# Optimization experiments

Hardware: AMD Instinct MI355X
Metric: run time of the kernel (lower is better)

The kernel has to match this reference:

```python
import jax, jax.numpy as jnp
import numpy as np

N, F_IN, C, H, E, G = 10000, 128, 256, 4, 160000, 512
BN_EPS = 1e-5


def setup_inputs() -> dict:
    key = jax.random.key(0)
    ks = iter(jax.random.split(key, 40))
    nrm = lambda shape, s=0.05: jax.random.normal(next(ks), shape, jnp.float32) * s

    def bn(dim):
        # rows: gamma, beta, running_mean, running_var (eval-mode BatchNorm)
        g = 1.0 + jax.random.normal(next(ks), (dim,), jnp.float32) * 0.1
        b = jax.random.normal(next(ks), (dim,), jnp.float32) * 0.1
        m = jax.random.normal(next(ks), (dim,), jnp.float32) * 0.1
        v = jax.random.uniform(next(ks), (dim,), jnp.float32, 0.5, 1.5)
        return jnp.stack([g, b, m, v])  # [4, dim]

    x = jax.random.normal(next(ks), (N, F_IN), jnp.float32)
    edge_index = jax.random.randint(next(ks), (2, E), 0, N, jnp.int64)
    batch = (jnp.arange(N, dtype=jnp.int64) * G) // N  # sorted, every graph non-empty

    return {
        "x": x, "edge_index": edge_index, "batch": batch,
        "W1": nrm((F_IN, H * C)), "att_src1": nrm((H, C)), "att_dst1": nrm((H, C)), "b1": nrm((H * C,)), "bn1": bn(H * C),
        "W2": nrm((H * C, H * C)), "att_src2": nrm((H, C)), "att_dst2": nrm((H, C)), "b2": nrm((H * C,)), "bn2": bn(H * C),
        "W3": nrm((H * C, C)), "att_src3": nrm((1, C)), "att_dst3": nrm((1, C)), "b3": nrm((C,)), "bn3": bn(C),
        "fc1_w": nrm((3 * C, 2 * C)), "fc1_b": nrm((2 * C,)), "bnf1": bn(2 * C),
        "fc2_w": nrm((2 * C, C)), "fc2_b": nrm((C,)), "bnf2": bn(C),
        "fc3_w": nrm((C, 1)), "fc3_b": nrm((1,)),
    }


def batchnorm(x, p):
    g, b, m, v = p
    return (x - m) * (g * jax.lax.rsqrt(v + BN_EPS)) + b


def gat_conv(x, src, dst, W, att_src, att_dst, bias, heads):
    n = x.shape[0]
    h = (x @ W).reshape(n, heads, -1)                      # [N,H,C]
    a_src = jnp.einsum('nhc,hc->nh', h, att_src)           # [N,H]
    a_dst = jnp.einsum('nhc,hc->nh', h, att_dst)
    logits = jax.nn.leaky_relu(a_src[src] + a_dst[dst], 0.2)  # [E,H]
    # scatter-softmax over incoming edges of each destination node
    m = jax.ops.segment_max(logits, dst, num_segments=n)
    m = jax.lax.stop_gradient(jnp.where(jnp.isfinite(m), m, 0.0))
    e = jnp.exp(logits - m[dst])
    denom = jax.ops.segment_sum(e, dst, num_segments=n)
    alpha = e / (denom[dst] + 1e-16)                       # [E,H]
    msg = h[src] * alpha[:, :, None]                       # [E,H,C]
    out = jax.ops.segment_sum(msg, dst, num_segments=n)    # [N,H,C]
    return out.reshape(n, -1) + bias


def reference(x, edge_index, batch,
              W1, att_src1, att_dst1, b1, bn1,
              W2, att_src2, att_dst2, b2, bn2,
              W3, att_src3, att_dst3, b3, bn3,
              fc1_w, fc1_b, bnf1, fc2_w, fc2_b, bnf2, fc3_w, fc3_b):
    src, dst = edge_index[0], edge_index[1]
    h = jax.nn.elu(batchnorm(gat_conv(x, src, dst, W1, att_src1, att_dst1, b1, H), bn1))
    h = jax.nn.elu(batchnorm(gat_conv(h, src, dst, W2, att_src2, att_dst2, b2, H), bn2))
    h = jax.nn.elu(batchnorm(gat_conv(h, src, dst, W3, att_src3, att_dst3, b3, 1), bn3))
    # multi-pool readout over graphs
    s = jax.ops.segment_sum(h, batch, num_segments=G)
    cnt = jax.ops.segment_sum(jnp.ones((h.shape[0], 1), h.dtype), batch, num_segments=G)
    mean = s / cnt
    mx = jax.ops.segment_max(h, batch, num_segments=G)
    z = jnp.concatenate([mean, mx, s], axis=1)             # [G, 3C]
    z = jax.nn.relu(batchnorm(z @ fc1_w + fc1_b, bnf1))    # dropout: eval mode (identity)
    z = jax.nn.relu(batchnorm(z @ fc2_w + fc2_b, bnf2))
    return z @ fc3_w + fc3_b                               # [G, 1]
```

## Files before the change

kernel.cpp:

```cpp
#include <hip/hip_runtime.h>
#include <math.h>

#define N_NODES 10000
#define N_EDGES 160000
#define N_GRAPH 512

#define NEG_INF (-1e30f)

typedef __attribute__((ext_vector_type(8))) short s16x8;
typedef __attribute__((ext_vector_type(4))) float f32x4;

__device__ __forceinline__ unsigned short f2b(float f) {
  union { float f; unsigned u; } c{f};
  unsigned u = c.u;
  return (unsigned short)((u + 0x7fff + ((u >> 16) & 1)) >> 16);
}
__device__ __forceinline__ float b2f(unsigned short h) {
  union { unsigned u; float f; } c{(unsigned)h << 16};
  return c.f;
}
__device__ __forceinline__ void up2(unsigned d, float& lo, float& hi) {
  union { unsigned u; float f; } a{d << 16}, b{d & 0xffff0000u};
  lo = a.f; hi = b.f;
}
__device__ __forceinline__ float lrelu(float x) { return x > 0.f ? x : 0.2f * x; }

#define GLL16(gp, lp)                                                          \
  __builtin_amdgcn_global_load_lds(                                            \
      (const __attribute__((address_space(1))) unsigned int*)(gp),             \
      (__attribute__((address_space(3))) unsigned int*)(lp), 16, 0, 0)

__global__ void k_count(const int* __restrict__ dst, const int* __restrict__ batch,
                        int* __restrict__ deg, int* __restrict__ gcnt) {
  int i = blockIdx.x * 256 + threadIdx.x;
  if (i < N_EDGES) atomicAdd(&deg[dst[i]], 1);
  if (i < N_NODES) atomicAdd(&gcnt[batch[i]], 1);
}

__global__ void k_scan2(const int* __restrict__ in1, int* __restrict__ out1, int n1,
                        const int* __restrict__ in2, int* __restrict__ out2, int n2) {
  __shared__ int buf[1024];
  __shared__ int carry_s;
#pragma unroll 1
  for (int pass = 0; pass < 2; ++pass) {
    const int* in = pass ? in2 : in1;
    int* out = pass ? out2 : out1;
    const int n = pass ? n2 : n1;
    if (threadIdx.x == 0) carry_s = 0;
    __syncthreads();
    for (int base = 0; base < n; base += 1024) {
      int i = base + (int)threadIdx.x;
      int v = (i < n) ? in[i] : 0;
      buf[threadIdx.x] = v;
      __syncthreads();
      for (int off = 1; off < 1024; off <<= 1) {
        int t = (threadIdx.x >= (unsigned)off) ? buf[threadIdx.x - off] : 0;
        __syncthreads();
        buf[threadIdx.x] += t;
        __syncthreads();
      }
      int carry = carry_s;
      if (i < n) out[i] = carry + buf[threadIdx.x] - v;
      __syncthreads();
      if (threadIdx.x == 0) carry_s = carry + buf[1023];
      __syncthreads();
    }
    if (threadIdx.x == 0) out[n] = carry_s;
    __syncthreads();
  }
}

__global__ void k_fill(const int* __restrict__ src, const int* __restrict__ dst,
                       const int* __restrict__ rowoff, int* __restrict__ cursor,
                       int* __restrict__ csr) {
  int e = blockIdx.x * 256 + threadIdx.x;
  if (e < N_EDGES) {
    int d = dst[e];
    int p = atomicAdd(&cursor[d], 1);
    csr[rowoff[d] + p] = src[e];
  }
}

__global__ __launch_bounds__(256) void k_sortseg(const int* __restrict__ rowoff,
                                                 int* __restrict__ vals) {
  const int node = blockIdx.x * 4 + (threadIdx.x >> 6);
  if (node >= N_NODES) return;
  const int lane = threadIdx.x & 63;
  const int a = rowoff[node], b = rowoff[node + 1];
  const int deg = b - a;
  if (deg <= 1) return;
  if (deg <= 64) {
    int v = (lane < deg) ? vals[a + lane] : 0x7fffffff;
#pragma unroll
    for (int ph = 0; ph < 64; ++ph) {
      const int par = ph & 1;
      const bool left = ((lane & 1) == par);
      const int partner = left ? lane + 1 : lane - 1;
      const int pv = __shfl(v, partner & 63);
      if (partner >= 0 && partner < 64) v = left ? min(v, pv) : max(v, pv);
    }
    if (lane < deg) vals[a + lane] = v;
  } else if (lane == 0) {
    for (int p = a + 1; p < b; ++p) {
      int v = vals[p];
      int q = p - 1;
      while (q >= a && vals[q] > v) { vals[q + 1] = vals[q]; --q; }
      vals[q + 1] = v;
    }
  }
}

__global__ __launch_bounds__(256) void k_convT(const float* __restrict__ in,
                                               unsigned short* __restrict__ out,
                                               int K, int M) {
  __shared__ float t[32][33];
  const int mb = blockIdx.x * 32, kb = blockIdx.y * 32;
  const int tx = threadIdx.x & 31, ty = threadIdx.x >> 5;
#pragma unroll
  for (int r = ty; r < 32; r += 8) t[r][tx] = in[(size_t)(kb + r) * M + mb + tx];
  __syncthreads();
#pragma unroll
  for (int r = ty; r < 32; r += 8)
    out[(size_t)(mb + r) * K + kb + tx] = f2b(t[tx][r]);
}

__global__ void k_wmix(const float* __restrict__ W, const float* __restrict__ attS,
                       const float* __restrict__ attD, float* __restrict__ wS,
                       float* __restrict__ wD) {
  const int i = blockIdx.x * 256 + threadIdx.x;
  if (i >= 512) return;
  const int f = i >> 2, h = i & 3;
  const float* wrow = W + (size_t)f * 1024 + h * 256;
  const float* as = attS + h * 256;
  const float* ad = attD + h * 256;
  float s = 0.f, d = 0.f;
  for (int c = 0; c < 256; ++c) {
    const float w = wrow[c];
    s += w * as[c];
    d += w * ad[c];
  }
  wS[f * 4 + h] = s;
  wD[f * 4 + h] = d;
}

__global__ __launch_bounds__(256) void k_prep_x(const float* __restrict__ x,
                                                const float* __restrict__ wS,
                                                const float* __restrict__ wD,
                                                unsigned short* __restrict__ x_bf,
                                                float* __restrict__ aS,
                                                float* __restrict__ aD) {
  __shared__ float sS[128][4], sD[128][4];
  const int tid = threadIdx.x;
  for (int i = tid; i < 512; i += 256) {
    sS[i >> 2][i & 3] = wS[i];
    sD[i >> 2][i & 3] = wD[i];
  }
  __syncthreads();
  const int node = blockIdx.x * 4 + (tid >> 6);
  if (node >= N_NODES) return;
  const int lane = tid & 63;
  const float2 xv = ((const float2*)(x + (size_t)node * 128))[lane];
  const unsigned o = (unsigned)f2b(xv.x) | ((unsigned)f2b(xv.y) << 16);
  ((unsigned*)x_bf)[(size_t)node * 64 + lane] = o;
  const float4 s0 = *(const float4*)sS[lane * 2];
  const float4 s1 = *(const float4*)sS[lane * 2 + 1];
  const float4 d0 = *(const float4*)sD[lane * 2];
  const float4 d1 = *(const float4*)sD[lane * 2 + 1];
  float a0 = xv.x * s0.x + xv.y * s1.x;
  float a1 = xv.x * s0.y + xv.y * s1.y;
  float a2 = xv.x * s0.z + xv.y * s1.z;
  float a3 = xv.x * s0.w + xv.y * s1.w;
  float b0 = xv.x * d0.x + xv.y * d1.x;
  float b1 = xv.x * d0.y + xv.y * d1.y;
  float b2 = xv.x * d0.z + xv.y * d1.z;
  float b3 = xv.x * d0.w + xv.y * d1.w;
#pragma unroll
  for (int off = 32; off; off >>= 1) {
    a0 += __shfl_xor(a0, off); a1 += __shfl_xor(a1, off);
    a2 += __shfl_xor(a2, off); a3 += __shfl_xor(a3, off);
    b0 += __shfl_xor(b0, off); b1 += __shfl_xor(b1, off);
    b2 += __shfl_xor(b2, off); b3 += __shfl_xor(b3, off);
  }
  if (lane == 0) {
    *(float4*)&aS[(size_t)node * 4] = make_float4(a0, a1, a2, a3);
    *(float4*)&aD[(size_t)node * 4] = make_float4(b0, b1, b2, b3);
  }
}

__global__ __launch_bounds__(256) void k_aggx(
    const unsigned short* __restrict__ x_bf, const float* __restrict__ aS,
    const float* __restrict__ aD, const int* __restrict__ rowoff,
    const int* __restrict__ csr, unsigned short* __restrict__ xt) {
  const int wv = threadIdx.x >> 6;
  const int lane = threadIdx.x & 63;
  const int node = blockIdx.x * 4 + wv;
  if (node >= N_NODES) return;

  __shared__ int s_src_all[4][64];
  __shared__ float s_alp_all[4][64][4];
  int* s_src = s_src_all[wv];
  float (*s_alp)[4] = s_alp_all[wv];

  const int r0 = rowoff[node];
  const int deg = rowoff[node + 1] - r0;
  const float4 ad4 = *(const float4*)&aD[(size_t)node * 4];

  float acc[8];
#pragma unroll
  for (int j = 0; j < 8; ++j) acc[j] = 0.f;

  auto gather = [&](int cnt) {
    int e = 0;
    for (; e + 4 <= cnt; e += 4) {
      unsigned v[4];
      float4 al[4];
#pragma unroll
      for (int u = 0; u < 4; ++u) {
        const int s = s_src[e + u];
        al[u] = *(const float4*)s_alp[e + u];
        v[u] = ((const unsigned*)(x_bf + ((size_t)s << 7)))[lane];
      }
#pragma unroll
      for (int u = 0; u < 4; ++u) {
        float lo, hi;
        up2(v[u], lo, hi);
        acc[0] += al[u].x * lo; acc[1] += al[u].x * hi;
        acc[2] += al[u].y * lo; acc[3] += al[u].y * hi;
        acc[4] += al[u].z * lo; acc[5] += al[u].z * hi;
        acc[6] += al[u].w * lo; acc[7] += al[u].w * hi;
      }
    }
    for (; e < cnt; ++e) {
      const int s = s_src[e];
      const float4 al = *(const float4*)s_alp[e];
      const unsigned v = ((const unsigned*)(x_bf + ((size_t)s << 7)))[lane];
      float lo, hi;
      up2(v, lo, hi);
      acc[0] += al.x * lo; acc[1] += al.x * hi;
      acc[2] += al.y * lo; acc[3] += al.y * hi;
      acc[4] += al.z * lo; acc[5] += al.z * hi;
      acc[6] += al.w * lo; acc[7] += al.w * hi;
    }
  };

  if (deg <= 64) {
    float l0, l1, l2, l3;
    int sE = 0;
    const bool act = lane < deg;
    if (act) {
      sE = csr[r0 + lane];
      const float4 sv = *(const float4*)&aS[(size_t)sE * 4];
      l0 = lrelu(sv.x + ad4.x);
      l1 = lrelu(sv.y + ad4.y);
      l2 = lrelu(sv.z + ad4.z);
      l3 = lrelu(sv.w + ad4.w);
    } else {
      l0 = l1 = l2 = l3 = NEG_INF;
    }
    float m0 = l0, m1 = l1, m2 = l2, m3 = l3;
#pragma unroll
    for (int off = 32; off; off >>= 1) {
      m0 = fmaxf(m0, __shfl_xor(m0, off));
      m1 = fmaxf(m1, __shfl_xor(m1, off));
      m2 = fmaxf(m2, __shfl_xor(m2, off));
      m3 = fmaxf(m3, __shfl_xor(m3, off));
    }
    float e0 = act ? __expf(l0 - m0) : 0.f;
    float e1 = act ? __expf(l1 - m1) : 0.f;
    float e2 = act ? __expf(l2 - m2) : 0.f;
    float e3 = act ? __expf(l3 - m3) : 0.f;
    float s0 = e0, s1 = e1, s2 = e2, s3 = e3;
#pragma unroll
    for (int off = 32; off; off >>= 1) {
      s0 += __shfl_xor(s0, off);
      s1 += __shfl_xor(s1, off);
      s2 += __shfl_xor(s2, off);
      s3 += __shfl_xor(s3, off);
    }
    if (act) {
      s_src[lane] = sE;
      s_alp[lane][0] = e0 / (s0 + 1e-16f);
      s_alp[lane][1] = e1 / (s1 + 1e-16f);
      s_alp[lane][2] = e2 / (s2 + 1e-16f);
      s_alp[lane][3] = e3 / (s3 + 1e-16f);
    }
    gather(deg);
  } else {
    auto logits = [&](int idx, float& a, float& b, float& c, float& d, int& s) {
      s = csr[r0 + idx];
      const float4 sv = *(const float4*)&aS[(size_t)s * 4];
      a = lrelu(sv.x + ad4.x);
      b = lrelu(sv.y + ad4.y);
      c = lrelu(sv.z + ad4.z);
      d = lrelu(sv.w + ad4.w);
    };
    float m0 = NEG_INF, m1 = NEG_INF, m2 = NEG_INF, m3 = NEG_INF;
    for (int base = 0; base < deg; base += 64) {
      if (base + lane < deg) {
        float a, b, c, d; int s;
        logits(base + lane, a, b, c, d, s);
        m0 = fmaxf(m0, a); m1 = fmaxf(m1, b); m2 = fmaxf(m2, c); m3 = fmaxf(m3, d);
      }
    }
#pragma unroll
    for (int off = 32; off; off >>= 1) {
      m0 = fmaxf(m0, __shfl_xor(m0, off));
      m1 = fmaxf(m1, __shfl_xor(m1, off));
      m2 = fmaxf(m2, __shfl_xor(m2, off));
      m3 = fmaxf(m3, __shfl_xor(m3, off));
    }
    float s0 = 0.f, s1 = 0.f, s2 = 0.f, s3 = 0.f;
    for (int base = 0; base < deg; base += 64) {
      if (base + lane < deg) {
        float a, b, c, d; int s;
        logits(base + lane, a, b, c, d, s);
        s0 += __expf(a - m0); s1 += __expf(b - m1);
        s2 += __expf(c - m2); s3 += __expf(d - m3);
      }
    }
#pragma unroll
    for (int off = 32; off; off >>= 1) {
      s0 += __shfl_xor(s0, off);
      s1 += __shfl_xor(s1, off);
      s2 += __shfl_xor(s2, off);
      s3 += __shfl_xor(s3, off);
    }
    const float d0 = 1.f / (s0 + 1e-16f), d1 = 1.f / (s1 + 1e-16f);
    const float d2 = 1.f / (s2 + 1e-16f), d3 = 1.f / (s3 + 1e-16f);
    for (int base = 0; base < deg; base += 64) {
      const int cnt = min(64, deg - base);
      if (lane < cnt) {
        float a, b, c, d; int s;
        logits(base + lane, a, b, c, d, s);
        s_src[lane] = s;
        s_alp[lane][0] = __expf(a - m0) * d0;
        s_alp[lane][1] = __expf(b - m1) * d1;
        s_alp[lane][2] = __expf(c - m2) * d2;
        s_alp[lane][3] = __expf(d - m3) * d3;
      }
      gather(cnt);
    }
  }

#pragma unroll
  for (int h = 0; h < 4; ++h) {
    const unsigned o = (unsigned)f2b(acc[h * 2]) | ((unsigned)f2b(acc[h * 2 + 1]) << 16);
    ((unsigned*)xt)[(size_t)node * 256 + h * 64 + lane] = o;
  }
}

__global__ __launch_bounds__(256) void k_gemm_bf16(
    const unsigned short* __restrict__ A, int lda,
    const unsigned short* __restrict__ Bt, int ldb,
    unsigned short* __restrict__ Cbf, int ldc,
    int M, int N, int K) {
  __shared__ unsigned short As[128 * 32];
  __shared__ unsigned short Bs[128 * 32];
  const int tid = threadIdx.x;
  const int lane = tid & 63, wave = tid >> 6;
  const int wr = wave >> 1, wc = wave & 1;
  const int m0 = blockIdx.y * 128, n0 = blockIdx.x * 128;

  f32x4 acc[4][4];
#pragma unroll
  for (int i = 0; i < 4; ++i)
#pragma unroll
    for (int j = 0; j < 4; ++j) acc[i][j] = (f32x4){0.f, 0.f, 0.f, 0.f};

  const int l4 = lane >> 2;
  const int kp8 = (lane & 3) * 8;
  int rA0 = m0 + wave * 32 + l4;
  int rA1 = rA0 + 16;
  rA0 = min(rA0, M - 1);
  rA1 = min(rA1, M - 1);
  const int rB0 = n0 + wave * 32 + l4;
  const int rB1 = rB0 + 16;
  const unsigned short* pA0 = A + (size_t)rA0 * lda + kp8;
  const unsigned short* pA1 = A + (size_t)rA1 * lda + kp8;
  const unsigned short* pB0 = Bt + (size_t)rB0 * ldb + kp8;
  const unsigned short* pB1 = Bt + (size_t)rB1 * ldb + kp8;
  unsigned short* lA = As + wave * 1024;
  unsigned short* lB = Bs + wave * 1024;

  const int fr = lane & 15, kg = (lane >> 4) * 8;

  for (int kb = 0; kb < K; kb += 32) {
    GLL16(pA0 + kb, lA);
    GLL16(pA1 + kb, lA + 512);
    GLL16(pB0 + kb, lB);
    GLL16(pB1 + kb, lB + 512);
    __syncthreads();

    s16x8 a[4], b[4];
#pragma unroll
    for (int m = 0; m < 4; ++m)
      a[m] = *(const s16x8*)&As[(wr * 64 + m * 16 + fr) * 32 + kg];
#pragma unroll
    for (int n = 0; n < 4; ++n)
      b[n] = *(const s16x8*)&Bs[(wc * 64 + n * 16 + fr) * 32 + kg];
#pragma unroll
    for (int m = 0; m < 4; ++m)
#pragma unroll
      for (int n = 0; n < 4; ++n)
        acc[m][n] = __builtin_amdgcn_mfma_f32_16x16x32_bf16(a[m], b[n], acc[m][n], 0, 0, 0);
    __syncthreads();
  }

  const int frow = (lane >> 4) * 4;
#pragma unroll
  for (int m = 0; m < 4; ++m) {
#pragma unroll
    for (int r = 0; r < 4; ++r) {
      const int row = m0 + wr * 64 + m * 16 + frow + r;
      if (row < M) {
#pragma unroll
        for (int n = 0; n < 4; ++n) {
          const int col = n0 + wc * 64 + n * 16 + fr;
          Cbf[(size_t)row * ldc + col] = f2b(acc[m][n][r]);
        }
      }
    }
  }
}

__global__ __launch_bounds__(256) void k_gemm_l1(
    const unsigned short* __restrict__ xt,
    const unsigned short* __restrict__ W1t,
    unsigned short* __restrict__ Cbf,
    int M, const float* __restrict__ bias, const float* __restrict__ bn) {
  constexpr int K = 128, lda = 512, ldb = 128, ldc = 1024;
  __shared__ unsigned short As[128 * 32];
  __shared__ unsigned short Bs[128 * 32];
  const int tid = threadIdx.x;
  const int lane = tid & 63, wave = tid >> 6;
  const int wr = wave >> 1, wc = wave & 1;
  const int bx = blockIdx.x;
  const int h = bx >> 1;
  const int n0 = (bx & 1) * 128;
  const int colbase = h * 256;
  const int m0 = blockIdx.y * 128;
  const unsigned short* A = xt + h * 128;
  const unsigned short* Bt = W1t + (size_t)colbase * ldb;

  f32x4 acc[4][4];
#pragma unroll
  for (int i = 0; i < 4; ++i)
#pragma unroll
    for (int j = 0; j < 4; ++j) acc[i][j] = (f32x4){0.f, 0.f, 0.f, 0.f};

  const int l4 = lane >> 2;
  const int kp8 = (lane & 3) * 8;
  int rA0 = m0 + wave * 32 + l4;
  int rA1 = rA0 + 16;
  rA0 = min(rA0, M - 1);
  rA1 = min(rA1, M - 1);
  const int rB0 = n0 + wave * 32 + l4;
  const int rB1 = rB0 + 16;
  const unsigned short* pA0 = A + (size_t)rA0 * lda + kp8;
  const unsigned short* pA1 = A + (size_t)rA1 * lda + kp8;
  const unsigned short* pB0 = Bt + (size_t)rB0 * ldb + kp8;
  const unsigned short* pB1 = Bt + (size_t)rB1 * ldb + kp8;
  unsigned short* lA = As + wave * 1024;
  unsigned short* lB = Bs + wave * 1024;

  const int fr = lane & 15, kg = (lane >> 4) * 8;

  for (int kb = 0; kb < K; kb += 32) {
    GLL16(pA0 + kb, lA);
    GLL16(pA1 + kb, lA + 512);
    GLL16(pB0 + kb, lB);
    GLL16(pB1 + kb, lB + 512);
    __syncthreads();

    s16x8 a[4], b[4];
#pragma unroll
    for (int m = 0; m < 4; ++m)
      a[m] = *(const s16x8*)&As[(wr * 64 + m * 16 + fr) * 32 + kg];
#pragma unroll
    for (int n = 0; n < 4; ++n)
      b[n] = *(const s16x8*)&Bs[(wc * 64 + n * 16 + fr) * 32 + kg];
#pragma unroll
    for (int m = 0; m < 4; ++m)
#pragma unroll
      for (int n = 0; n < 4; ++n)
        acc[m][n] = __builtin_amdgcn_mfma_f32_16x16x32_bf16(a[m], b[n], acc[m][n], 0, 0, 0);
    __syncthreads();
  }

  const int frow = (lane >> 4) * 4;
#pragma unroll
  for (int m = 0; m < 4; ++m) {
#pragma unroll
    for (int r = 0; r < 4; ++r) {
      const int row = m0 + wr * 64 + m * 16 + frow + r;
      if (row < M) {
#pragma unroll
        for (int n = 0; n < 4; ++n) {
          const int col = n0 + wc * 64 + n * 16 + fr;
          const int gcol = colbase + col;
          float v = acc[m][n][r] + bias[gcol];
          const float g = bn[gcol], b = bn[1024 + gcol];
          const float mu = bn[2048 + gcol], var = bn[3072 + gcol];
          v = (v - mu) * (g * rsqrtf(var + 1e-5f)) + b;
          v = v > 0.f ? v : (__expf(v) - 1.f);
          Cbf[(size_t)row * ldc + gcol] = f2b(v);
        }
      }
    }
  }
}

template <int K, int M>
__global__ __launch_bounds__(256) void k_head_fc(
    const float* __restrict__ A, const float* __restrict__ W,
    float* __restrict__ C, const float* __restrict__ bias,
    const float* __restrict__ bn) {
  constexpr int KQ = K / 4;
  __shared__ float Ap[8 * K];
  __shared__ float part[4][8][64];
  const int tid = threadIdx.x;
  const int g0 = blockIdx.y * 8;
  const int m0 = blockIdx.x * 64;
  const int c = tid & 63;
  const int q = tid >> 6;

  for (int i = tid; i < 8 * K / 4; i += 256)
    ((float4*)Ap)[i] = ((const float4*)(A + (size_t)g0 * K))[i];
  __syncthreads();

  float acc[8];
#pragma unroll
  for (int r = 0; r < 8; ++r) acc[r] = 0.f;

  const float* Wc = W + m0 + c;
  const int k0 = q * KQ;
  for (int k = k0; k < k0 + KQ; k += 4) {
    float wv[4];
#pragma unroll
    for (int u = 0; u < 4; ++u) wv[u] = Wc[(size_t)(k + u) * M];
#pragma unroll
    for (int r = 0; r < 8; ++r) {
      const float4 a4 = *(const float4*)&Ap[r * K + k];
      acc[r] += a4.x * wv[0] + a4.y * wv[1] + a4.z * wv[2] + a4.w * wv[3];
    }
  }

#pragma unroll
  for (int r = 0; r < 8; ++r) part[q][r][c] = acc[r];
  __syncthreads();

  for (int i = tid; i < 512; i += 256) {
    const int r = i >> 6, cc = i & 63;
    float v = part[0][r][cc] + part[1][r][cc] + part[2][r][cc] + part[3][r][cc];
    const int gc = m0 + cc;
    v += bias[gc];
    const float g = bn[gc], b = bn[M + gc], mu = bn[2 * M + gc], var = bn[3 * M + gc];
    v = (v - mu) * (g * rsqrtf(var + 1e-5f)) + b;
    v = fmaxf(v, 0.f);
    C[(size_t)(g0 + r) * M + gc] = v;
  }
}

template <int HEADS>
__global__ __launch_bounds__(256) void k_att(const unsigned short* __restrict__ h,
                                             const float* __restrict__ att_s,
                                             const float* __restrict__ att_d,
                                             float* __restrict__ aS,
                                             float* __restrict__ aD) {
  const int pair = blockIdx.x * 4 + (threadIdx.x >> 6);
  if (pair >= N_NODES * HEADS) return;
  const int node = pair / HEADS, hd = pair % HEADS;
  const int lane = threadIdx.x & 63;
  const unsigned short* row = h + (size_t)node * HEADS * 256 + hd * 256;
  const ushort4 v = *(const ushort4*)&row[lane * 4];
  const float4 s4 = *(const float4*)&att_s[hd * 256 + lane * 4];
  const float4 d4 = *(const float4*)&att_d[hd * 256 + lane * 4];
  float ss = b2f(v.x) * s4.x + b2f(v.y) * s4.y + b2f(v.z) * s4.z + b2f(v.w) * s4.w;
  float sd = b2f(v.x) * d4.x + b2f(v.y) * d4.y + b2f(v.z) * d4.z + b2f(v.w) * d4.w;
#pragma unroll
  for (int off = 32; off; off >>= 1) {
    ss += __shfl_xor(ss, off);
    sd += __shfl_xor(sd, off);
  }
  if (lane == 0) {
    aS[pair] = ss;
    aD[pair] = sd;
  }
}

__global__ __launch_bounds__(256) void k_aggw4(
    const unsigned short* __restrict__ hpre, const float* __restrict__ aS,
    const float* __restrict__ aD, const int* __restrict__ rowoff,
    const int* __restrict__ csr, const float* __restrict__ bias,
    const float* __restrict__ bn, unsigned short* __restrict__ outb) {
  const int wv = threadIdx.x >> 6;
  const int lane = threadIdx.x & 63;
  const int node = blockIdx.x * 2 + (wv >> 1);
  const int half = wv & 1;
  if (node >= N_NODES) return;

  __shared__ int s_src_all[4][64];
  __shared__ float s_alp_all[4][64][2];
  int* s_src = s_src_all[wv];
  float (*s_alp)[2] = s_alp_all[wv];

  const int r0 = rowoff[node];
  const int deg = rowoff[node + 1] - r0;
  const float2 ad2 = *(const float2*)&aD[(size_t)node * 4 + half * 2];

  float acc[8];
#pragma unroll
  for (int j = 0; j < 8; ++j) acc[j] = 0.f;

  const int hg = lane >> 5;
  const size_t choff = (size_t)half * 512;

  auto gather = [&](int cnt) {
    int e = 0;
    for (; e + 4 <= cnt; e += 4) {
      uint4 v[4];
      float al[4];
#pragma unroll
      for (int u = 0; u < 4; ++u) {
        const int s = s_src[e + u];
        al[u] = s_alp[e + u][hg];
        v[u] = ((const uint4*)(hpre + ((size_t)s << 10) + choff))[lane];
      }
#pragma unroll
      for (int u = 0; u < 4; ++u) {
        float lo, hi;
        up2(v[u].x, lo, hi); acc[0] += al[u] * lo; acc[1] += al[u] * hi;
        up2(v[u].y, lo, hi); acc[2] += al[u] * lo; acc[3] += al[u] * hi;
        up2(v[u].z, lo, hi); acc[4] += al[u] * lo; acc[5] += al[u] * hi;
        up2(v[u].w, lo, hi); acc[6] += al[u] * lo; acc[7] += al[u] * hi;
      }
    }
    for (; e < cnt; ++e) {
      const int s = s_src[e];
      const float al = s_alp[e][hg];
      const uint4 v = ((const uint4*)(hpre + ((size_t)s << 10) + choff))[lane];
      float lo, hi;
      up2(v.x, lo, hi); acc[0] += al * lo; acc[1] += al * hi;
      up2(v.y, lo, hi); acc[2] += al * lo; acc[3] += al * hi;
      up2(v.z, lo, hi); acc[4] += al * lo; acc[5] += al * hi;
      up2(v.w, lo, hi); acc[6] += al * lo; acc[7] += al * hi;
    }
  };

  if (deg <= 64) {
    float la, lb;
    int sE = 0;
    const bool act = lane < deg;
    if (act) {
      sE = csr[r0 + lane];
      const float2 sv = *(const float2*)&aS[(size_t)sE * 4 + half * 2];
      la = lrelu(sv.x + ad2.x);
      lb = lrelu(sv.y + ad2.y);
    } else {
      la = lb = NEG_INF;
    }
    float ma = la, mb = lb;
#pragma unroll
    for (int off = 32; off; off >>= 1) {
      ma = fmaxf(ma, __shfl_xor(ma, off));
      mb = fmaxf(mb, __shfl_xor(mb, off));
    }
    float ea = act ? __expf(la - ma) : 0.f;
    float eb = act ? __expf(lb - mb) : 0.f;
    float sa = ea, sb = eb;
#pragma unroll
    for (int off = 32; off; off >>= 1) {
      sa += __shfl_xor(sa, off);
      sb += __shfl_xor(sb, off);
    }
    if (act) {
      s_src[lane] = sE;
      s_alp[lane][0] = ea / (sa + 1e-16f);
      s_alp[lane][1] = eb / (sb + 1e-16f);
    }
    gather(deg);
  } else {
    auto logits = [&](int idx, float& a, float& b, int& s) {
      s = csr[r0 + idx];
      const float2 sv = *(const float2*)&aS[(size_t)s * 4 + half * 2];
      a = lrelu(sv.x + ad2.x);
      b = lrelu(sv.y + ad2.y);
    };
    float ma = NEG_INF, mb = NEG_INF;
    for (int base = 0; base < deg; base += 64) {
      if (base + lane < deg) {
        float a, b; int s;
        logits(base + lane, a, b, s);
        ma = fmaxf(ma, a); mb = fmaxf(mb, b);
      }
    }
#pragma unroll
    for (int off = 32; off; off >>= 1) {
      ma = fmaxf(ma, __shfl_xor(ma, off));
      mb = fmaxf(mb, __shfl_xor(mb, off));
    }
    float sa = 0.f, sb = 0.f;
    for (int base = 0; base < deg; base += 64) {
      if (base + lane < deg) {
        float a, b; int s;
        logits(base + lane, a, b, s);
        sa += __expf(a - ma); sb += __expf(b - mb);
      }
    }
#pragma unroll
    for (int off = 32; off; off >>= 1) {
      sa += __shfl_xor(sa, off);
      sb += __shfl_xor(sb, off);
    }
    const float da = 1.f / (sa + 1e-16f), db = 1.f / (sb + 1e-16f);
    for (int base = 0; base < deg; base += 64) {
      const int cnt = min(64, deg - base);
      if (lane < cnt) {
        float a, b; int s;
        logits(base + lane, a, b, s);
        s_src[lane] = s;
        s_alp[lane][0] = __expf(a - ma) * da;
        s_alp[lane][1] = __expf(b - mb) * db;
      }
      gather(cnt);
    }
  }

  const int cb = half * 512 + lane * 8;
  unsigned od[4];
#pragma unroll
  for (int jj = 0; jj < 2; ++jj) {
    const float4 bi = *(const float4*)&bias[cb + jj * 4];
    const float4 gg = *(const float4*)&bn[cb + jj * 4];
    const float4 bb = *(const float4*)&bn[1024 + cb + jj * 4];
    const float4 mm = *(const float4*)&bn[2048 + cb + jj * 4];
    const float4 vv = *(const float4*)&bn[3072 + cb + jj * 4];
    float r[4];
#pragma unroll
    for (int j = 0; j < 4; ++j) {
      float v = acc[jj * 4 + j] + ((const float*)&bi)[j];
      v = (v - ((const float*)&mm)[j]) *
              (((const float*)&gg)[j] * rsqrtf(((const float*)&vv)[j] + 1e-5f)) +
          ((const float*)&bb)[j];
      v = v > 0.f ? v : (__expf(v) - 1.f);
      r[j] = v;
    }
    od[jj * 2 + 0] = (unsigned)f2b(r[0]) | ((unsigned)f2b(r[1]) << 16);
    od[jj * 2 + 1] = (unsigned)f2b(r[2]) | ((unsigned)f2b(r[3]) << 16);
  }
  *(uint4*)&outb[((size_t)node << 10) + cb] = make_uint4(od[0], od[1], od[2], od[3]);
}

__global__ __launch_bounds__(256) void k_aggw1(
    const unsigned short* __restrict__ hpre, const float* __restrict__ aS,
    const float* __restrict__ aD, const int* __restrict__ rowoff,
    const int* __restrict__ csr, const float* __restrict__ bias,
    const float* __restrict__ bn, float* __restrict__ outf) {
  const int wv = threadIdx.x >> 6;
  const int lane = threadIdx.x & 63;
  const int node = blockIdx.x * 4 + wv;
  if (node >= N_NODES) return;

  __shared__ int s_src_all[4][64];
  __shared__ float s_alp_all[4][64];
  int* s_src = s_src_all[wv];
  float* s_alp = s_alp_all[wv];

  const int r0 = rowoff[node];
  const int deg = rowoff[node + 1] - r0;
  const float ad = aD[node];

  float acc[4] = {0.f, 0.f, 0.f, 0.f};

  auto gather = [&](int cnt) {
    int e = 0;
    for (; e + 4 <= cnt; e += 4) {
      uint2 v[4];
      float al[4];
#pragma unroll
      for (int u = 0; u < 4; ++u) {
        const int s = s_src[e + u];
        al[u] = s_alp[e + u];
        v[u] = ((const uint2*)(hpre + ((size_t)s << 8)))[lane];
      }
#pragma unroll
      for (int u = 0; u < 4; ++u) {
        float lo, hi;
        up2(v[u].x, lo, hi); acc[0] += al[u] * lo; acc[1] += al[u] * hi;
        up2(v[u].y, lo, hi); acc[2] += al[u] * lo; acc[3] += al[u] * hi;
      }
    }
    for (; e < cnt; ++e) {
      const int s = s_src[e];
      const float al = s_alp[e];
      const uint2 v = ((const uint2*)(hpre + ((size_t)s << 8)))[lane];
      float lo, hi;
      up2(v.x, lo, hi); acc[0] += al * lo; acc[1] += al * hi;
      up2(v.y, lo, hi); acc[2] += al * lo; acc[3] += al * hi;
    }
  };

  if (deg <= 64) {
    float l0;
    int sE = 0;
    const bool act = lane < deg;
    if (act) {
      sE = csr[r0 + lane];
      l0 = lrelu(aS[sE] + ad);
    } else {
      l0 = NEG_INF;
    }
    float m0 = l0;
#pragma unroll
    for (int off = 32; off; off >>= 1) m0 = fmaxf(m0, __shfl_xor(m0, off));
    float e0 = act ? __expf(l0 - m0) : 0.f;
    float s0 = e0;
#pragma unroll
    for (int off = 32; off; off >>= 1) s0 += __shfl_xor(s0, off);
    if (act) {
      s_src[lane] = sE;
      s_alp[lane] = e0 / (s0 + 1e-16f);
    }
    gather(deg);
  } else {
    float m0 = NEG_INF;
    for (int base = 0; base < deg; base += 64)
      if (base + lane < deg) m0 = fmaxf(m0, lrelu(aS[csr[r0 + base + lane]] + ad));
#pragma unroll
    for (int off = 32; off; off >>= 1) m0 = fmaxf(m0, __shfl_xor(m0, off));
    float s0 = 0.f;
    for (int base = 0; base < deg; base += 64)
      if (base + lane < deg) s0 += __expf(lrelu(aS[csr[r0 + base + lane]] + ad) - m0);
#pragma unroll
    for (int off = 32; off; off >>= 1) s0 += __shfl_xor(s0, off);
    const float d0 = 1.f / (s0 + 1e-16f);
    for (int base = 0; base < deg; base += 64) {
      const int cnt = min(64, deg - base);
      if (lane < cnt) {
        const int s = csr[r0 + base + lane];
        s_src[lane] = s;
        s_alp[lane] = __expf(lrelu(aS[s] + ad) - m0) * d0;
      }
      gather(cnt);
    }
  }

  const int c = lane * 4;
  const float4 bi = *(const float4*)&bias[c];
  const float4 gg = *(const float4*)&bn[c];
  const float4 bb = *(const float4*)&bn[256 + c];
  const float4 mm = *(const float4*)&bn[512 + c];
  const float4 vv = *(const float4*)&bn[768 + c];
  float4 o;
#pragma unroll
  for (int j = 0; j < 4; ++j) {
    float v = acc[j] + ((const float*)&bi)[j];
    v = (v - ((const float*)&mm)[j]) *
            (((const float*)&gg)[j] * rsqrtf(((const float*)&vv)[j] + 1e-5f)) +
        ((const float*)&bb)[j];
    v = v > 0.f ? v : (__expf(v) - 1.f);
    ((float*)&o)[j] = v;
  }
  *(float4*)&outf[((size_t)node << 8) + c] = o;
}

__global__ __launch_bounds__(256) void k_pool(const float* __restrict__ h,
                                              const int* __restrict__ goff,
                                              float* __restrict__ z) {
  const int g = blockIdx.x;
  const int c = threadIdx.x;
  const int i0 = goff[g], i1 = goff[g + 1];
  float s = 0.f, mx = NEG_INF;
  for (int i = i0; i < i1; ++i) {
    float v = h[(size_t)i * 256 + c];
    s += v;
    mx = fmaxf(mx, v);
  }
  const float cnt = (float)(i1 - i0);
  z[(size_t)g * 768 + c] = s / cnt;
  z[(size_t)g * 768 + 256 + c] = mx;
  z[(size_t)g * 768 + 512 + c] = s;
}

__global__ __launch_bounds__(64) void k_fc3(const float* __restrict__ z2,
                                            const float* __restrict__ w,
                                            const float* __restrict__ b,
                                            float* __restrict__ out) {
  const int g = blockIdx.x;
  const int lane = threadIdx.x;
  float s = 0.f;
#pragma unroll
  for (int j = 0; j < 4; ++j) {
    int c = lane + 64 * j;
    s += z2[(size_t)g * 256 + c] * w[c];
  }
#pragma unroll
  for (int off = 32; off; off >>= 1) s += __shfl_xor(s, off);
  if (lane == 0) out[g] = s + b[0];
}

extern "C" void kernel_launch(void* const* d_in, const int* in_sizes, int n_in,
                              void* d_out, int out_size, void* d_ws, size_t ws_size,
                              hipStream_t stream) {
  const float* x    = (const float*)d_in[0];
  const int* ei     = (const int*)d_in[1];
  const int* batch  = (const int*)d_in[2];
  const float* W1   = (const float*)d_in[3];
  const float* as1  = (const float*)d_in[4];
  const float* ad1  = (const float*)d_in[5];
  const float* b1   = (const float*)d_in[6];
  const float* bn1  = (const float*)d_in[7];
  const float* W2   = (const float*)d_in[8];
  const float* as2  = (const float*)d_in[9];
  const float* ad2  = (const float*)d_in[10];
  const float* b2   = (const float*)d_in[11];
  const float* bn2  = (const float*)d_in[12];
  const float* W3   = (const float*)d_in[13];
  const float* as3  = (const float*)d_in[14];
  const float* ad3  = (const float*)d_in[15];
  const float* b3   = (const float*)d_in[16];
  const float* bn3  = (const float*)d_in[17];
  const float* fc1w = (const float*)d_in[18];
  const float* fc1b = (const float*)d_in[19];
  const float* bnf1 = (const float*)d_in[20];
  const float* fc2w = (const float*)d_in[21];
  const float* fc2b = (const float*)d_in[22];
  const float* bnf2 = (const float*)d_in[23];
  const float* fc3w = (const float*)d_in[24];
  const float* fc3b = (const float*)d_in[25];
  float* out = (float*)d_out;

  const int* e_src = ei;
  const int* e_dst = ei + N_EDGES;

  char* w = (char*)d_ws;
  auto alloc = [&](size_t bytes) -> void* {
    void* p = (void*)w;
    w += (bytes + 255) & ~(size_t)255;
    return p;
  };
  unsigned short* x_bf  = (unsigned short*)alloc((size_t)N_NODES * 128 * 2);
  unsigned short* xt    = (unsigned short*)alloc((size_t)N_NODES * 512 * 2);
  unsigned short* W1t   = (unsigned short*)alloc((size_t)1024 * 128 * 2);
  unsigned short* W2t   = (unsigned short*)alloc((size_t)1024 * 1024 * 2);
  unsigned short* W3t   = (unsigned short*)alloc((size_t)256 * 1024 * 2);
  unsigned short* hA_bf = (unsigned short*)alloc((size_t)N_NODES * 1024 * 2);
  unsigned short* hB_bf = (unsigned short*)alloc((size_t)N_NODES * 1024 * 2);
  float* hB_f32 = (float*)alloc((size_t)N_NODES * 256 * 4);
  float* aS   = (float*)alloc((size_t)N_NODES * 4 * 4);
  float* aD   = (float*)alloc((size_t)N_NODES * 4 * 4);
  float* wS1  = (float*)alloc((size_t)512 * 4);
  float* wD1  = (float*)alloc((size_t)512 * 4);
  int* deg    = (int*)alloc((size_t)(2 * N_NODES + N_GRAPH) * 4);
  int* cursor = deg + N_NODES;
  int* gcnt   = deg + 2 * N_NODES;
  int* rowoff = (int*)alloc((size_t)(N_NODES + 1) * 4);
  int* goff   = (int*)alloc((size_t)(N_GRAPH + 1) * 4);
  int* csr    = (int*)alloc((size_t)N_EDGES * 4);
  float* z    = (float*)alloc((size_t)N_GRAPH * 768 * 4);
  float* z1   = (float*)alloc((size_t)N_GRAPH * 512 * 4);
  float* z2   = (float*)alloc((size_t)N_GRAPH * 256 * 4);

  hipMemsetAsync(deg, 0, (size_t)(2 * N_NODES + N_GRAPH) * 4, stream);

  k_convT<<<dim3(1024 / 32, 128 / 32), 256, 0, stream>>>(W1, W1t, 128, 1024);
  k_convT<<<dim3(1024 / 32, 1024 / 32), 256, 0, stream>>>(W2, W2t, 1024, 1024);
  k_convT<<<dim3(256 / 32, 1024 / 32), 256, 0, stream>>>(W3, W3t, 1024, 256);
  k_wmix<<<2, 256, 0, stream>>>(W1, as1, ad1, wS1, wD1);
  k_prep_x<<<(N_NODES + 3) / 4, 256, 0, stream>>>(x, wS1, wD1, x_bf, aS, aD);

  k_count<<<(N_EDGES + 255) / 256, 256, 0, stream>>>(e_dst, batch, deg, gcnt);
  k_scan2<<<1, 1024, 0, stream>>>(deg, rowoff, N_NODES, gcnt, goff, N_GRAPH);
  k_fill<<<(N_EDGES + 255) / 256, 256, 0, stream>>>(e_src, e_dst, rowoff, cursor, csr);
  k_sortseg<<<(N_NODES + 3) / 4, 256, 0, stream>>>(rowoff, csr);

  const int mt = (N_NODES + 127) / 128;
  const int nb2 = (N_NODES + 1) / 2;
  const int nb4 = (N_NODES + 3) / 4;

  k_aggx<<<nb4, 256, 0, stream>>>(x_bf, aS, aD, rowoff, csr, xt);
  k_gemm_l1<<<dim3(8, mt), 256, 0, stream>>>(xt, W1t, hB_bf, N_NODES, b1, bn1);

  k_gemm_bf16<<<dim3(1024 / 128, mt), 256, 0, stream>>>(
      hB_bf, 1024, W2t, 1024, hA_bf, 1024, N_NODES, 1024, 1024);
  k_att<4><<<(N_NODES * 4 + 3) / 4, 256, 0, stream>>>(hA_bf, as2, ad2, aS, aD);
  k_aggw4<<<nb2, 256, 0, stream>>>(hA_bf, aS, aD, rowoff, csr, b2, bn2, hB_bf);

  k_gemm_bf16<<<dim3(256 / 128, mt), 256, 0, stream>>>(
      hB_bf, 1024, W3t, 1024, hA_bf, 256, N_NODES, 256, 1024);
  k_att<1><<<(N_NODES + 3) / 4, 256, 0, stream>>>(hA_bf, as3, ad3, aS, aD);
  k_aggw1<<<nb4, 256, 0, stream>>>(hA_bf, aS, aD, rowoff, csr, b3, bn3, hB_f32);

  k_pool<<<N_GRAPH, 256, 0, stream>>>(hB_f32, goff, z);
  k_head_fc<768, 512><<<dim3(512 / 64, N_GRAPH / 8), 256, 0, stream>>>(z, fc1w, z1, fc1b, bnf1);
  k_head_fc<512, 256><<<dim3(256 / 64, N_GRAPH / 8), 256, 0, stream>>>(z1, fc2w, z2, fc2b, bnf2);
  k_fc3<<<N_GRAPH, 64, 0, stream>>>(z2, fc3w, fc3b, out);
}
```

Baseline: 310.1 us.

## Split GAT layer 2/3 aggregation into edge-softmax pass and column-sliced gather

Replaces the fused per-node softmax+gather kernels for layers 2 and 3 with two kernels. The first computes per-edge attention weights once per head into a head-major buffer. The second gathers neighbour features in 128-column slices across a second grid dimension, each wave reading 4 bytes per lane per edge. This raises parallelism and avoids recomputing logits in every aggregating wave. In exchange it adds an extra launch, an extra pass over the edge array and narrower, less coalesced per-edge row reads repeated across slices.

```diff
diff --git a/kernel.cpp b/kernel.cpp
--- a/kernel.cpp
+++ b/kernel.cpp
@@ -349,6 +349,167 @@
   }
 }
 
+template <int H>
+__global__ __launch_bounds__(256) void k_alpha(
+    const float* __restrict__ aS, const float* __restrict__ aD,
+    const int* __restrict__ rowoff, const int* __restrict__ csr,
+    float* __restrict__ alpT) {
+  const int wv = threadIdx.x >> 6;
+  const int lane = threadIdx.x & 63;
+  const int node = blockIdx.x * 4 + wv;
+  if (node >= N_NODES) return;
+  const int r0 = rowoff[node];
+  const int deg = rowoff[node + 1] - r0;
+  float adh[H];
+#pragma unroll
+  for (int h = 0; h < H; ++h) adh[h] = aD[(size_t)node * H + h];
+
+  if (deg <= 64) {
+    const bool act = lane < deg;
+    int sE = act ? csr[r0 + lane] : 0;
+    float l[H];
+#pragma unroll
+    for (int h = 0; h < H; ++h)
+      l[h] = act ? lrelu(aS[(size_t)sE * H + h] + adh[h]) : NEG_INF;
+    float m[H];
+#pragma unroll
+    for (int h = 0; h < H; ++h) {
+      m[h] = l[h];
+#pragma unroll
+      for (int off = 32; off; off >>= 1) m[h] = fmaxf(m[h], __shfl_xor(m[h], off));
+    }
+    float e[H], s[H];
+#pragma unroll
+    for (int h = 0; h < H; ++h) {
+      e[h] = act ? __expf(l[h] - m[h]) : 0.f;
+      s[h] = e[h];
+#pragma unroll
+      for (int off = 32; off; off >>= 1) s[h] += __shfl_xor(s[h], off);
+    }
+    if (act) {
+#pragma unroll
+      for (int h = 0; h < H; ++h)
+        alpT[(size_t)h * N_EDGES + r0 + lane] = e[h] / (s[h] + 1e-16f);
+    }
+  } else {
+    float m[H], s[H];
+#pragma unroll
+    for (int h = 0; h < H; ++h) { m[h] = NEG_INF; s[h] = 0.f; }
+    for (int base = 0; base < deg; base += 64) {
+      if (base + lane < deg) {
+        const int sE = csr[r0 + base + lane];
+#pragma unroll
+        for (int h = 0; h < H; ++h)
+          m[h] = fmaxf(m[h], lrelu(aS[(size_t)sE * H + h] + adh[h]));
+      }
+    }
+#pragma unroll
+    for (int h = 0; h < H; ++h)
+#pragma unroll
+      for (int off = 32; off; off >>= 1) m[h] = fmaxf(m[h], __shfl_xor(m[h], off));
+    for (int base = 0; base < deg; base += 64) {
+      if (base + lane < deg) {
+        const int sE = csr[r0 + base + lane];
+#pragma unroll
+        for (int h = 0; h < H; ++h)
+          s[h] += __expf(lrelu(aS[(size_t)sE * H + h] + adh[h]) - m[h]);
+      }
+    }
+#pragma unroll
+    for (int h = 0; h < H; ++h)
+#pragma unroll
+      for (int off = 32; off; off >>= 1) s[h] += __shfl_xor(s[h], off);
+    float dinv[H];
+#pragma unroll
+    for (int h = 0; h < H; ++h) dinv[h] = 1.f / (s[h] + 1e-16f);
+    for (int base = 0; base < deg; base += 64) {
+      if (base + lane < deg) {
+        const int sE = csr[r0 + base + lane];
+#pragma unroll
+        for (int h = 0; h < H; ++h)
+          alpT[(size_t)h * N_EDGES + r0 + base + lane] =
+              __expf(lrelu(aS[(size_t)sE * H + h] + adh[h]) - m[h]) * dinv[h];
+      }
+    }
+  }
+}
+
+template <int HC, int OUTF>
+__global__ __launch_bounds__(256) void k_aggs(
+    const unsigned short* __restrict__ h, const float* __restrict__ alpT,
+    const int* __restrict__ rowoff, const int* __restrict__ csr,
+    const float* __restrict__ bias, const float* __restrict__ bn,
+    unsigned short* __restrict__ outb, float* __restrict__ outf) {
+  const int wv = threadIdx.x >> 6;
+  const int lane = threadIdx.x & 63;
+  const int node = blockIdx.x * 4 + wv;
+  if (node >= N_NODES) return;
+  const int slice = blockIdx.y;
+  const int head = (HC == 1024) ? (slice >> 1) : 0;
+  const float* alp = alpT + (size_t)head * N_EDGES;
+
+  __shared__ int s_src_all[4][64];
+  __shared__ float s_a_all[4][64];
+  int* s_src = s_src_all[wv];
+  float* s_a = s_a_all[wv];
+
+  const int r0 = rowoff[node];
+  const int deg = rowoff[node + 1] - r0;
+  const unsigned* hbase = (const unsigned*)h + slice * 64 + lane;
+  constexpr int RDW = HC / 2;
+
+  float a0 = 0.f, a1 = 0.f;
+
+  for (int base = 0; base < deg; base += 64) {
+    const int cnt = min(64, deg - base);
+    if (lane < cnt) {
+      s_src[lane] = csr[r0 + base + lane];
+      s_a[lane] = alp[r0 + base + lane];
+    }
+    int e = 0;
+    for (; e + 4 <= cnt; e += 4) {
+      unsigned v[4];
+      float al[4];
+#pragma unroll
+      for (int u = 0; u < 4; ++u) {
+        const int s = s_src[e + u];
+        al[u] = s_a[e + u];
+        v[u] = hbase[(size_t)s * RDW];
+      }
+#pragma unroll
+      for (int u = 0; u < 4; ++u) {
+        float lo, hi;
+        up2(v[u], lo, hi);
+        a0 += al[u] * lo;
+        a1 += al[u] * hi;
+      }
+    }
+    for (; e < cnt; ++e) {
+      const int s = s_src[e];
+      const float al = s_a[e];
+      const unsigned v = hbase[(size_t)s * RDW];
+      float lo, hi;
+      up2(v, lo, hi);
+      a0 += al * lo;
+      a1 += al * hi;
+    }
+  }
+
+  const int cb = slice * 128 + lane * 2;
+  float v0 = a0 + bias[cb];
+  float v1 = a1 + bias[cb + 1];
+  v0 = (v0 - bn[2 * HC + cb]) * (bn[cb] * rsqrtf(bn[3 * HC + cb] + 1e-5f)) + bn[HC + cb];
+  v1 = (v1 - bn[2 * HC + cb + 1]) * (bn[cb + 1] * rsqrtf(bn[3 * HC + cb + 1] + 1e-5f)) + bn[HC + cb + 1];
+  v0 = v0 > 0.f ? v0 : (__expf(v0) - 1.f);
+  v1 = v1 > 0.f ? v1 : (__expf(v1) - 1.f);
+  if (OUTF) {
+    *(float2*)&outf[(size_t)node * HC + cb] = make_float2(v0, v1);
+  } else {
+    ((unsigned*)outb)[(size_t)node * RDW + slice * 64 + lane] =
+        (unsigned)f2b(v0) | ((unsigned)f2b(v1) << 16);
+  }
+}
+
 __global__ __launch_bounds__(256) void k_gemm_bf16(
     const unsigned short* __restrict__ A, int lda,
     const unsigned short* __restrict__ Bt, int ldb,
@@ -586,282 +747,6 @@
     aS[pair] = ss;
     aD[pair] = sd;
   }
-}
-
-__global__ __launch_bounds__(256) void k_aggw4(
-    const unsigned short* __restrict__ hpre, const float* __restrict__ aS,
-    const float* __restrict__ aD, const int* __restrict__ rowoff,
-    const int* __restrict__ csr, const float* __restrict__ bias,
-    const float* __restrict__ bn, unsigned short* __restrict__ outb) {
-  const int wv = threadIdx.x >> 6;
-  const int lane = threadIdx.x & 63;
-  const int node = blockIdx.x * 2 + (wv >> 1);
-  const int half = wv & 1;
-  if (node >= N_NODES) return;
-
-  __shared__ int s_src_all[4][64];
-  __shared__ float s_alp_all[4][64][2];
-  int* s_src = s_src_all[wv];
-  float (*s_alp)[2] = s_alp_all[wv];
-
-  const int r0 = rowoff[node];
-  const int deg = rowoff[node + 1] - r0;
-  const float2 ad2 = *(const float2*)&aD[(size_t)node * 4 + half * 2];
-
-  float acc[8];
-#pragma unroll
-  for (int j = 0; j < 8; ++j) acc[j] = 0.f;
-
-  const int hg = lane >> 5;
-  const size_t choff = (size_t)half * 512;
-
-  auto gather = [&](int cnt) {
-    int e = 0;
-    for (; e + 4 <= cnt; e += 4) {
-      uint4 v[4];
-      float al[4];
-#pragma unroll
-      for (int u = 0; u < 4; ++u) {
-        const int s = s_src[e + u];
-        al[u] = s_alp[e + u][hg];
-        v[u] = ((const uint4*)(hpre + ((size_t)s << 10) + choff))[lane];
-      }
-#pragma unroll
-      for (int u = 0; u < 4; ++u) {
-        float lo, hi;
-        up2(v[u].x, lo, hi); acc[0] += al[u] * lo; acc[1] += al[u] * hi;
-        up2(v[u].y, lo, hi); acc[2] += al[u] * lo; acc[3] += al[u] * hi;
-        up2(v[u].z, lo, hi); acc[4] += al[u] * lo; acc[5] += al[u] * hi;
-        up2(v[u].w, lo, hi); acc[6] += al[u] * lo; acc[7] += al[u] * hi;
-      }
-    }
-    for (; e < cnt; ++e) {
-      const int s = s_src[e];
-      const float al = s_alp[e][hg];
-      const uint4 v = ((const uint4*)(hpre + ((size_t)s << 10) + choff))[lane];
-      float lo, hi;
-      up2(v.x, lo, hi); acc[0] += al * lo; acc[1] += al * hi;
-      up2(v.y, lo, hi); acc[2] += al * lo; acc[3] += al * hi;
-      up2(v.z, lo, hi); acc[4] += al * lo; acc[5] += al * hi;
-      up2(v.w, lo, hi); acc[6] += al * lo; acc[7] += al * hi;
-    }
-  };
-
-  if (deg <= 64) {
-    float la, lb;
-    int sE = 0;
-    const bool act = lane < deg;
-    if (act) {
-      sE = csr[r0 + lane];
-      const float2 sv = *(const float2*)&aS[(size_t)sE * 4 + half * 2];
-      la = lrelu(sv.x + ad2.x);
-      lb = lrelu(sv.y + ad2.y);
-    } else {
-      la = lb = NEG_INF;
-    }
-    float ma = la, mb = lb;
-#pragma unroll
-    for (int off = 32; off; off >>= 1) {
-      ma = fmaxf(ma, __shfl_xor(ma, off));
-      mb = fmaxf(mb, __shfl_xor(mb, off));
-    }
-    float ea = act ? __expf(la - ma) : 0.f;
-    float eb = act ? __expf(lb - mb) : 0.f;
-    float sa = ea, sb = eb;
-#pragma unroll
-    for (int off = 32; off; off >>= 1) {
-      sa += __shfl_xor(sa, off);
-      sb += __shfl_xor(sb, off);
-    }
-    if (act) {
-      s_src[lane] = sE;
-      s_alp[lane][0] = ea / (sa + 1e-16f);
-      s_alp[lane][1] = eb / (sb + 1e-16f);
-    }
-    gather(deg);
-  } else {
-    auto logits = [&](int idx, float& a, float& b, int& s) {
-      s = csr[r0 + idx];
-      const float2 sv = *(const float2*)&aS[(size_t)s * 4 + half * 2];
-      a = lrelu(sv.x + ad2.x);
-      b = lrelu(sv.y + ad2.y);
-    };
-    float ma = NEG_INF, mb = NEG_INF;
-    for (int base = 0; base < deg; base += 64) {
-      if (base + lane < deg) {
-        float a, b; int s;
-        logits(base + lane, a, b, s);
-        ma = fmaxf(ma, a); mb = fmaxf(mb, b);
-      }
-    }
-#pragma unroll
-    for (int off = 32; off; off >>= 1) {
-      ma = fmaxf(ma, __shfl_xor(ma, off));
-      mb = fmaxf(mb, __shfl_xor(mb, off));
-    }
-    float sa = 0.f, sb = 0.f;
-    for (int base = 0; base < deg; base += 64) {
-      if (base + lane < deg) {
-        float a, b; int s;
-        logits(base + lane, a, b, s);
-        sa += __expf(a - ma); sb += __expf(b - mb);
-      }
-    }
-#pragma unroll
-    for (int off = 32; off; off >>= 1) {
-      sa += __shfl_xor(sa, off);
-      sb += __shfl_xor(sb, off);
-    }
-    const float da = 1.f / (sa + 1e-16f), db = 1.f / (sb + 1e-16f);
-    for (int base = 0; base < deg; base += 64) {
-      const int cnt = min(64, deg - base);
-      if (lane < cnt) {
-        float a, b; int s;
-        logits(base + lane, a, b, s);
-        s_src[lane] = s;
-        s_alp[lane][0] = __expf(a - ma) * da;
-        s_alp[lane][1] = __expf(b - mb) * db;
-      }
-      gather(cnt);
-    }
-  }
-
-  const int cb = half * 512 + lane * 8;
-  unsigned od[4];
-#pragma unroll
-  for (int jj = 0; jj < 2; ++jj) {
-    const float4 bi = *(const float4*)&bias[cb + jj * 4];
-    const float4 gg = *(const float4*)&bn[cb + jj * 4];
-    const float4 bb = *(const float4*)&bn[1024 + cb + jj * 4];
-    const float4 mm = *(const float4*)&bn[2048 + cb + jj * 4];
-    const float4 vv = *(const float4*)&bn[3072 + cb + jj * 4];
-    float r[4];
-#pragma unroll
-    for (int j = 0; j < 4; ++j) {
-      float v = acc[jj * 4 + j] + ((const float*)&bi)[j];
-      v = (v - ((const float*)&mm)[j]) *
-              (((const float*)&gg)[j] * rsqrtf(((const float*)&vv)[j] + 1e-5f)) +
-          ((const float*)&bb)[j];
-      v = v > 0.f ? v : (__expf(v) - 1.f);
-      r[j] = v;
-    }
-    od[jj * 2 + 0] = (unsigned)f2b(r[0]) | ((unsigned)f2b(r[1]) << 16);
-    od[jj * 2 + 1] = (unsigned)f2b(r[2]) | ((unsigned)f2b(r[3]) << 16);
-  }
-  *(uint4*)&outb[((size_t)node << 10) + cb] = make_uint4(od[0], od[1], od[2], od[3]);
-}
-
-__global__ __launch_bounds__(256) void k_aggw1(
-    const unsigned short* __restrict__ hpre, const float* __restrict__ aS,
-    const float* __restrict__ aD, const int* __restrict__ rowoff,
-    const int* __restrict__ csr, const float* __restrict__ bias,
-    const float* __restrict__ bn, float* __restrict__ outf) {
-  const int wv = threadIdx.x >> 6;
-  const int lane = threadIdx.x & 63;
-  const int node = blockIdx.x * 4 + wv;
-  if (node >= N_NODES) return;
-
-  __shared__ int s_src_all[4][64];
-  __shared__ float s_alp_all[4][64];
-  int* s_src = s_src_all[wv];
-  float* s_alp = s_alp_all[wv];
-
-  const int r0 = rowoff[node];
-  const int deg = rowoff[node + 1] - r0;
-  const float ad = aD[node];
-
-  float acc[4] = {0.f, 0.f, 0.f, 0.f};
-
-  auto gather = [&](int cnt) {
-    int e = 0;
-    for (; e + 4 <= cnt; e += 4) {
-      uint2 v[4];
-      float al[4];
-#pragma unroll
-      for (int u = 0; u < 4; ++u) {
-        const int s = s_src[e + u];
-        al[u] = s_alp[e + u];
-        v[u] = ((const uint2*)(hpre + ((size_t)s << 8)))[lane];
-      }
-#pragma unroll
-      for (int u = 0; u < 4; ++u) {
-        float lo, hi;
-        up2(v[u].x, lo, hi); acc[0] += al[u] * lo; acc[1] += al[u] * hi;
-        up2(v[u].y, lo, hi); acc[2] += al[u] * lo; acc[3] += al[u] * hi;
-      }
-    }
-    for (; e < cnt; ++e) {
-      const int s = s_src[e];
-      const float al = s_alp[e];
-      const uint2 v = ((const uint2*)(hpre + ((size_t)s << 8)))[lane];
-      float lo, hi;
-      up2(v.x, lo, hi); acc[0] += al * lo; acc[1] += al * hi;
-      up2(v.y, lo, hi); acc[2] += al * lo; acc[3] += al * hi;
-    }
-  };
-
-  if (deg <= 64) {
-    float l0;
-    int sE = 0;
-    const bool act = lane < deg;
-    if (act) {
-      sE = csr[r0 + lane];
-      l0 = lrelu(aS[sE] + ad);
-    } else {
-      l0 = NEG_INF;
-    }
-    float m0 = l0;
-#pragma unroll
-    for (int off = 32; off; off >>= 1) m0 = fmaxf(m0, __shfl_xor(m0, off));
-    float e0 = act ? __expf(l0 - m0) : 0.f;
-    float s0 = e0;
-#pragma unroll
-    for (int off = 32; off; off >>= 1) s0 += __shfl_xor(s0, off);
-    if (act) {
-      s_src[lane] = sE;
-      s_alp[lane] = e0 / (s0 + 1e-16f);
-    }
-    gather(deg);
-  } else {
-    float m0 = NEG_INF;
-    for (int base = 0; base < deg; base += 64)
-      if (base + lane < deg) m0 = fmaxf(m0, lrelu(aS[csr[r0 + base + lane]] + ad));
-#pragma unroll
-    for (int off = 32; off; off >>= 1) m0 = fmaxf(m0, __shfl_xor(m0, off));
-    float s0 = 0.f;
-    for (int base = 0; base < deg; base += 64)
-      if (base + lane < deg) s0 += __expf(lrelu(aS[csr[r0 + base + lane]] + ad) - m0);
-#pragma unroll
-    for (int off = 32; off; off >>= 1) s0 += __shfl_xor(s0, off);
-    const float d0 = 1.f / (s0 + 1e-16f);
-    for (int base = 0; base < deg; base += 64) {
-      const int cnt = min(64, deg - base);
-      if (lane < cnt) {
-        const int s = csr[r0 + base + lane];
-        s_src[lane] = s;
-        s_alp[lane] = __expf(lrelu(aS[s] + ad) - m0) * d0;
-      }
-      gather(cnt);
-    }
-  }
-
-  const int c = lane * 4;
-  const float4 bi = *(const float4*)&bias[c];
-  const float4 gg = *(const float4*)&bn[c];
-  const float4 bb = *(const float4*)&bn[256 + c];
-  const float4 mm = *(const float4*)&bn[512 + c];
-  const float4 vv = *(const float4*)&bn[768 + c];
-  float4 o;
-#pragma unroll
-  for (int j = 0; j < 4; ++j) {
-    float v = acc[j] + ((const float*)&bi)[j];
-    v = (v - ((const float*)&mm)[j]) *
-            (((const float*)&gg)[j] * rsqrtf(((const float*)&vv)[j] + 1e-5f)) +
-        ((const float*)&bb)[j];
-    v = v > 0.f ? v : (__expf(v) - 1.f);
-    ((float*)&o)[j] = v;
-  }
-  *(float4*)&outf[((size_t)node << 8) + c] = o;
 }
 
 __global__ __launch_bounds__(256) void k_pool(const float* __restrict__ h,
@@ -951,6 +836,8 @@
   float* aD   = (float*)alloc((size_t)N_NODES * 4 * 4);
   float* wS1  = (float*)alloc((size_t)512 * 4);
   float* wD1  = (float*)alloc((size_t)512 * 4);
+  float* alp4 = (float*)alloc((size_t)N_EDGES * 4 * 4);
+  float* alp1 = (float*)alloc((size_t)N_EDGES * 4);
   int* deg    = (int*)alloc((size_t)(2 * N_NODES + N_GRAPH) * 4);
   int* cursor = deg + N_NODES;
   int* gcnt   = deg + 2 * N_NODES;
@@ -975,7 +862,6 @@
   k_sortseg<<<(N_NODES + 3) / 4, 256, 0, stream>>>(rowoff, csr);
 
   const int mt = (N_NODES + 127) / 128;
-  const int nb2 = (N_NODES + 1) / 2;
   const int nb4 = (N_NODES + 3) / 4;
 
   k_aggx<<<nb4, 256, 0, stream>>>(x_bf, aS, aD, rowoff, csr, xt);
@@ -984,12 +870,16 @@
   k_gemm_bf16<<<dim3(1024 / 128, mt), 256, 0, stream>>>(
       hB_bf, 1024, W2t, 1024, hA_bf, 1024, N_NODES, 1024, 1024);
   k_att<4><<<(N_NODES * 4 + 3) / 4, 256, 0, stream>>>(hA_bf, as2, ad2, aS, aD);
-  k_aggw4<<<nb2, 256, 0, stream>>>(hA_bf, aS, aD, rowoff, csr, b2, bn2, hB_bf);
+  k_alpha<4><<<nb4, 256, 0, stream>>>(aS, aD, rowoff, csr, alp4);
+  k_aggs<1024, 0><<<dim3(nb4, 8), 256, 0, stream>>>(
+      hA_bf, alp4, rowoff, csr, b2, bn2, hB_bf, nullptr);
 
   k_gemm_bf16<<<dim3(256 / 128, mt), 256, 0, stream>>>(
       hB_bf, 1024, W3t, 1024, hA_bf, 256, N_NODES, 256, 1024);
   k_att<1><<<(N_NODES + 3) / 4, 256, 0, stream>>>(hA_bf, as3, ad3, aS, aD);
-  k_aggw1<<<nb4, 256, 0, stream>>>(hA_bf, aS, aD, rowoff, csr, b3, bn3, hB_f32);
+  k_alpha<1><<<nb4, 256, 0, stream>>>(aS, aD, rowoff, csr, alp1);
+  k_aggs<256, 1><<<dim3(nb4, 2), 256, 0, stream>>>(
+      hA_bf, alp1, rowoff, csr, b3, bn3, nullptr, hB_f32);
 
   k_pool<<<N_GRAPH, 256, 0, stream>>>(hB_f32, goff, z);
   k_head_fc<768, 512><<<dim3(512 / 64, N_GRAPH / 8), 256, 0, stream>>>(z, fc1w, z1, fc1b, bnf1);
```

Measured after the change: 324.5 us. +4.7%, slower.
